# Optimization experiments

Hardware: AMD Instinct MI355X
Metric: run time of the kernel (lower is better)

Reference implementation:

```python
import jax, jax.numpy as jnp
import numpy as np

MULS = [128, 64, 32, 16]   # multiplicity per l (same for in and out)
LS   = [0, 1, 2, 3]
ALPHA = 0.2  # SmoothLeakyReLU negative slope (Equiformer)


def smooth_leaky_relu(x):
    # ((1+a)/2)*x + ((1-a)/2)*x*(2*sigmoid(x)-1)
    return ((1 + ALPHA) / 2) * x + ((1 - ALPHA) / 2) * x * (2 * jax.nn.sigmoid(x) - 1)


def setup_inputs() -> dict:
    key = jax.random.key(0)
    ks = jax.random.split(key, 6)
    N = 100000
    L_in = sum(m * (2 * l + 1) for m, l in zip(MULS, LS))  # 592
    inp = {"x": jax.random.normal(ks[0], (N, L_in), dtype=jnp.float32)}
    for i, m in enumerate(MULS):
        bound = 1.0 / np.sqrt(m)
        inp[f"w{i}"] = jax.random.uniform(ks[1 + i], (m, m), minval=-bound, maxval=bound, dtype=jnp.float32)
    inp["b0"] = jax.random.normal(ks[5], (MULS[0],), dtype=jnp.float32)
    inp["b1"] = jnp.zeros((MULS[1],), jnp.float32)
    inp["b2"] = jnp.zeros((MULS[2],), jnp.float32)
    inp["b3"] = jnp.zeros((MULS[3],), jnp.float32)
    return inp


def reference(x, w0, w1, w2, w3, b0, b1, b2, b3):
    ws = [w0, w1, w2, w3]
    bs = [b0, b1, b2, b3]
    N = x.shape[0]
    outs = []
    start = 0
    for i, (mul, l) in enumerate(zip(MULS, LS)):
        d = 2 * l + 1
        seg = x[:, start:start + mul * d].reshape(N, mul, d)  # [N, mul, 2l+1]
        out = jnp.einsum('om,nmd->nod', ws[i], seg) + bs[i][None, :, None]
        if l == 0:
            out = smooth_leaky_relu(out)
        outs.append(out.reshape(N, -1))
        start += mul * d
    return jnp.concatenate(outs, axis=1)  # [N, 592]
```

## Files before the change

### kernel.cpp

```cpp
#include <hip/hip_runtime.h>
#include <math.h>

#define BLOCK 512
#define TILE_R 64
#define LIN 592
#define LDS_FLOATS 12480

__device__ __forceinline__ float slr(float v) {
    float s = 1.0f / (1.0f + __expf(-v));
    return v * (0.2f + 0.8f * s);
}

template<int MUL, int D, int C0, int MB, bool ACT>
__device__ __forceinline__ void seg_compute(
    float* __restrict__ xs,
    const float* __restrict__ x,
    const float* __restrict__ w,
    const float* __restrict__ b,
    float* __restrict__ out,
    int n0, int N, int tid, int lane, int wv)
{
    constexpr int SEGC = MUL * D;
    constexpr int S    = SEGC + 1;
    constexpr int OPW  = MUL / 8;
    constexpr int TR1  = TILE_R + 1;

    constexpr int CH = SEGC / 4;
    constexpr int F4 = TILE_R * CH;
    #pragma unroll 1
    for (int i = tid; i < F4; i += BLOCK) {
        int r  = i / CH;
        int cb = i - r * CH;
        int gr = n0 + r;
        float4 v = make_float4(0.f, 0.f, 0.f, 0.f);
        if (gr < N) v = *(const float4*)(x + (size_t)gr * LIN + C0 + cb * 4);
        float* dst = xs + r * S + cb * 4;
        dst[0] = v.x; dst[1] = v.y; dst[2] = v.z; dst[3] = v.w;
    }
    __syncthreads();

    float acc[OPW * D];
    #pragma unroll
    for (int oo = 0; oo < OPW; ++oo) {
        float bv = b[wv * OPW + oo];
        #pragma unroll
        for (int j = 0; j < D; ++j) acc[oo * D + j] = bv;
    }

    const float* xrow = xs + lane * S;
    #pragma unroll 1
    for (int mb = 0; mb < MUL; mb += MB) {
        float xv[MB * D];
        #pragma unroll
        for (int k = 0; k < MB * D; ++k) xv[k] = xrow[mb * D + k];
        #pragma unroll
        for (int oo = 0; oo < OPW; ++oo) {
            const float* wr = w + (wv * OPW + oo) * MUL + mb;
            #pragma unroll
            for (int mm = 0; mm < MB; ++mm) {
                float wval = wr[mm];
                #pragma unroll
                for (int j = 0; j < D; ++j)
                    acc[oo * D + j] = fmaf(wval, xv[mm * D + j], acc[oo * D + j]);
            }
        }
    }

    if (ACT) {
        #pragma unroll
        for (int i = 0; i < OPW * D; ++i) acc[i] = slr(acc[i]);
    }

    __syncthreads();
    {
        int c0w = wv * (OPW * D);
        #pragma unroll
        for (int i = 0; i < OPW * D; ++i)
            xs[(c0w + i) * TR1 + lane] = acc[i];
    }
    __syncthreads();

    constexpr int TOT = TILE_R * SEGC;
    #pragma unroll 1
    for (int i = tid; i < TOT; i += BLOCK) {
        int r = i / SEGC;
        int c = i - r * SEGC;
        int row = n0 + r;
        if (row < N)
            out[(size_t)row * LIN + C0 + c] = xs[c * TR1 + r];
    }
}

__global__ __launch_bounds__(BLOCK, 6)
void irreps_kernel(const float* __restrict__ x,
                   const float* __restrict__ w0, const float* __restrict__ w1,
                   const float* __restrict__ w2, const float* __restrict__ w3,
                   const float* __restrict__ b0, const float* __restrict__ b1,
                   const float* __restrict__ b2, const float* __restrict__ b3,
                   float* __restrict__ out, int N)
{
    __shared__ float xs[LDS_FLOATS];
    int tid  = threadIdx.x;
    int lane = tid & 63;
    int wv   = __builtin_amdgcn_readfirstlane(tid >> 6);
    int n0   = blockIdx.x * TILE_R;

    switch (blockIdx.y) {
    case 0: seg_compute<128, 1,   0, 16, true >(xs, x, w0, b0, out, n0, N, tid, lane, wv); break;
    case 1: seg_compute< 64, 3, 128,  8, false>(xs, x, w1, b1, out, n0, N, tid, lane, wv); break;
    case 2: seg_compute< 32, 5, 320,  4, false>(xs, x, w2, b2, out, n0, N, tid, lane, wv); break;
    default:seg_compute< 16, 7, 480,  4, false>(xs, x, w3, b3, out, n0, N, tid, lane, wv); break;
    }
}

extern "C" void kernel_launch(void* const* d_in, const int* in_sizes, int n_in,
                              void* d_out, int out_size, void* d_ws, size_t ws_size,
                              hipStream_t stream) {
    const float* x  = (const float*)d_in[0];
    const float* w0 = (const float*)d_in[1];
    const float* w1 = (const float*)d_in[2];
    const float* w2 = (const float*)d_in[3];
    const float* w3 = (const float*)d_in[4];
    const float* b0 = (const float*)d_in[5];
    const float* b1 = (const float*)d_in[6];
    const float* b2 = (const float*)d_in[7];
    const float* b3 = (const float*)d_in[8];
    float* out = (float*)d_out;

    int N = in_sizes[0] / LIN;
    dim3 grid((N + TILE_R - 1) / TILE_R, 4);
    irreps_kernel<<<grid, BLOCK, 0, stream>>>(x, w0, w1, w2, w3,
                                              b0, b1, b2, b3, out, N);
}
```

Before: 484.9 us.

## Use XOR-swizzled float4 LDS layout for tile staging and vectorized stores

Replaces the padded scalar LDS layout with a row-major float4 layout whose 16-byte chunk index is XOR-swizzled by row, so staging writes, per-lane row reads, and result writes can all use 128-bit LDS accesses while keeping bank conflicts low. The output write-back now goes row-major through the same layout, which lets global stores be float4 instead of scalar. The aim is fewer LDS instructions and better-coalesced wide global stores on this memory-bound kernel. The odd-width segment (l=3, 14 floats per wave) falls back to scalar swizzled writes.

```diff
diff --git a/kernel.cpp b/kernel.cpp
--- a/kernel.cpp
+++ b/kernel.cpp
@@ -4,7 +4,7 @@
 #define BLOCK 512
 #define TILE_R 64
 #define LIN 592
-#define LDS_FLOATS 12480
+#define LDS_FLOATS (64 * 48 * 4)
 
 __device__ __forceinline__ float slr(float v) {
     float s = 1.0f / (1.0f + __expf(-v));
@@ -21,21 +21,20 @@
     int n0, int N, int tid, int lane, int wv)
 {
     constexpr int SEGC = MUL * D;
-    constexpr int S    = SEGC + 1;
+    constexpr int CH   = SEGC / 4;
+    constexpr int CHP  = (CH + 7) & ~7;
     constexpr int OPW  = MUL / 8;
-    constexpr int TR1  = TILE_R + 1;
+    float4* xs4 = (float4*)xs;
 
-    constexpr int CH = SEGC / 4;
     constexpr int F4 = TILE_R * CH;
     #pragma unroll 1
     for (int i = tid; i < F4; i += BLOCK) {
         int r  = i / CH;
-        int cb = i - r * CH;
+        int c4 = i - r * CH;
         int gr = n0 + r;
         float4 v = make_float4(0.f, 0.f, 0.f, 0.f);
-        if (gr < N) v = *(const float4*)(x + (size_t)gr * LIN + C0 + cb * 4);
-        float* dst = xs + r * S + cb * 4;
-        dst[0] = v.x; dst[1] = v.y; dst[2] = v.z; dst[3] = v.w;
+        if (gr < N) v = *(const float4*)(x + (size_t)gr * LIN + C0 + c4 * 4);
+        xs4[r * CHP + (c4 ^ (r & 7))] = v;
     }
     __syncthreads();
 
@@ -47,12 +46,16 @@
         for (int j = 0; j < D; ++j) acc[oo * D + j] = bv;
     }
 
-    const float* xrow = xs + lane * S;
+    const int rbase = lane * CHP;
+    const int sw    = lane & 7;
     #pragma unroll 1
     for (int mb = 0; mb < MUL; mb += MB) {
         float xv[MB * D];
         #pragma unroll
-        for (int k = 0; k < MB * D; ++k) xv[k] = xrow[mb * D + k];
+        for (int k4 = 0; k4 < (MB * D) / 4; ++k4) {
+            float4 v = xs4[rbase + (((mb * D) / 4 + k4) ^ sw)];
+            xv[4*k4+0] = v.x; xv[4*k4+1] = v.y; xv[4*k4+2] = v.z; xv[4*k4+3] = v.w;
+        }
         #pragma unroll
         for (int oo = 0; oo < OPW; ++oo) {
             const float* wr = w + (wv * OPW + oo) * MUL + mb;
@@ -72,22 +75,32 @@
     }
 
     __syncthreads();
-    {
-        int c0w = wv * (OPW * D);
+    if constexpr ((OPW * D) % 4 == 0) {
+        constexpr int K4 = (OPW * D) / 4;
+        int c0 = wv * K4;
         #pragma unroll
-        for (int i = 0; i < OPW * D; ++i)
-            xs[(c0w + i) * TR1 + lane] = acc[i];
+        for (int k4 = 0; k4 < K4; ++k4) {
+            float4 v = make_float4(acc[4*k4], acc[4*k4+1], acc[4*k4+2], acc[4*k4+3]);
+            xs4[rbase + ((c0 + k4) ^ sw)] = v;
+        }
+    } else {
+        int c0 = wv * (OPW * D);
+        #pragma unroll
+        for (int i = 0; i < OPW * D; ++i) {
+            int c = c0 + i;
+            xs[(rbase + ((c >> 2) ^ sw)) * 4 + (c & 3)] = acc[i];
+        }
     }
     __syncthreads();
 
-    constexpr int TOT = TILE_R * SEGC;
     #pragma unroll 1
-    for (int i = tid; i < TOT; i += BLOCK) {
-        int r = i / SEGC;
-        int c = i - r * SEGC;
+    for (int i = tid; i < F4; i += BLOCK) {
+        int r  = i / CH;
+        int c4 = i - r * CH;
         int row = n0 + r;
+        float4 v = xs4[r * CHP + (c4 ^ (r & 7))];
         if (row < N)
-            out[(size_t)row * LIN + C0 + c] = xs[c * TR1 + r];
+            *(float4*)(out + (size_t)row * LIN + C0 + c4 * 4) = v;
     }
 }
 
```

Measured after the change: 484.3 us. No clear change (-0.1%).
